# Optimization experiments

Hardware: AMD Instinct MI355X
Metric: run time of the kernel (lower is better)

Reference implementation:

```python
import jax, jax.numpy as jnp
import numpy as np
from jax import lax

# WaveNet constants (canonical values, see shape_source)
AUDIO_C = 256      # AUDIO_CHANNEL_SIZE (mu-law classes)
RES_C   = 64       # ONE_CONV_RESIDUAL_OUT_CHANNELS
FG_C    = 64       # FILTER_GATE_OUT_CHANNELS
SKIP_C  = 256      # ONE_CONV_SKIP_OUT_CHANNELS
K       = 2        # FILTER_GATE_KERNEL_SIZE
BLOCK_N_LAYERS = 10
N_BLOCKS = 2
L = BLOCK_N_LAYERS * N_BLOCKS  # 20 layers
B, T = 4, 16384


def causal_conv(x, w, b, dilation):
    # x: [B,C,T], w: [O,I,K] -> left-padded (causal) dilated conv, output [B,O,T]
    pad = dilation * (K - 1)
    y = lax.conv_general_dilated(x, w, window_strides=(1,), padding=[(pad, 0)],
                                 rhs_dilation=(dilation,),
                                 dimension_numbers=('NCH', 'OIH', 'NCH'))
    return y + b[None, :, None]


def conv1x1(x, w, b):
    # x: [B,C,T], w: [O,C], b: [O]
    return jnp.einsum('oc,bct->bot', w, x) + b[None, :, None]


def setup_inputs() -> dict:
    key = jax.random.key(0)
    ks = jax.random.split(key, 16)
    s = 0.1
    return {
        'x':       jax.random.normal(ks[0], (B, AUDIO_C, T), dtype=jnp.float32),
        'pre_w':   jax.random.normal(ks[1], (RES_C, AUDIO_C), dtype=jnp.float32) * s,
        'pre_b':   jnp.zeros((RES_C,), dtype=jnp.float32),
        'filt_w':  jax.random.normal(ks[2], (L, FG_C, RES_C, K), dtype=jnp.float32) * s,
        'filt_b':  jnp.zeros((L, FG_C), dtype=jnp.float32),
        'gate_w':  jax.random.normal(ks[3], (L, FG_C, RES_C, K), dtype=jnp.float32) * s,
        'gate_b':  jnp.zeros((L, FG_C), dtype=jnp.float32),
        'res_w':   jax.random.normal(ks[4], (L, RES_C, FG_C), dtype=jnp.float32) * s,
        'res_b':   jnp.zeros((L, RES_C), dtype=jnp.float32),
        'skip_w':  jax.random.normal(ks[5], (L, SKIP_C, FG_C), dtype=jnp.float32) * s,
        'skip_b':  jnp.zeros((L, SKIP_C), dtype=jnp.float32),
        'pp1_w':   jax.random.normal(ks[6], (SKIP_C, SKIP_C), dtype=jnp.float32) * s,
        'pp1_b':   jnp.zeros((SKIP_C,), dtype=jnp.float32),
        'pp2_w':   jax.random.normal(ks[7], (AUDIO_C, SKIP_C), dtype=jnp.float32) * s,
        'pp2_b':   jnp.zeros((AUDIO_C,), dtype=jnp.float32),
    }


def reference(x, pre_w, pre_b, filt_w, filt_b, gate_w, gate_b,
              res_w, res_b, skip_w, skip_b, pp1_w, pp1_b, pp2_w, pp2_b):
    h = conv1x1(x, pre_w, pre_b)                       # [B,RES_C,T]
    skip_sum = jnp.zeros((x.shape[0], SKIP_C, x.shape[2]), dtype=x.dtype)
    for i in range(L):                                  # fixed small layer count
        d = 2 ** (i % BLOCK_N_LAYERS)
        wf = causal_conv(h, filt_w[i], filt_b[i], d)
        wg = causal_conv(h, gate_w[i], gate_b[i], d)
        z = jnp.tanh(wf) * jax.nn.sigmoid(wg)           # gated activation unit
        skip_sum = skip_sum + conv1x1(z, skip_w[i], skip_b[i])
        h = h + conv1x1(z, res_w[i], res_b[i])          # residual (dense) stream
    out = conv1x1(jax.nn.relu(skip_sum), pp1_w, pp1_b)  # skip post-processing
    out = conv1x1(jax.nn.relu(out), pp2_w, pp2_b)
    return out                                           # [B,AUDIO_C,T]
```

## Files before the change

kernel.cpp:

```cpp
#include <hip/hip_runtime.h>

#define T_LEN   16384
#define B_SZ    4
#define AUDIO_C 256
#define RES_C   64
#define SKIP_C  256
#define L_LAYERS 20

typedef unsigned short u16;
using bf16x8 = __attribute__((ext_vector_type(8))) __bf16;
using f32x4  = __attribute__((ext_vector_type(4))) float;

__device__ __forceinline__ u16 f2bf(float x){
    union { float f; unsigned u; } v; v.f = x;
    return (u16)((v.u + 0x7FFFu + ((v.u >> 16) & 1u)) >> 16);
}
__device__ __forceinline__ unsigned cvt2(float a, float b){
    union { __bf16 h[2]; unsigned u; } r;
    r.h[0] = (__bf16)a; r.h[1] = (__bf16)b;
    return r.u;
}
__device__ __forceinline__ float bflo(unsigned u){ union{unsigned q; float f;} v; v.q = u << 16; return v.f; }
__device__ __forceinline__ float bfhi(unsigned u){ union{unsigned q; float f;} v; v.q = u & 0xffff0000u; return v.f; }
__device__ __forceinline__ f32x4 mfma16(uint4 a, uint4 b, f32x4 c){
    return __builtin_amdgcn_mfma_f32_16x16x32_bf16(
        __builtin_bit_cast(bf16x8, a), __builtin_bit_cast(bf16x8, b), c, 0, 0, 0);
}
__device__ __forceinline__ int xcd_swz1k(int bid){ return (bid & 7) * 128 + (bid >> 3); }
__device__ __forceinline__ void bar_lgkm(){
    asm volatile("s_waitcnt lgkmcnt(0)" ::: "memory");
    __builtin_amdgcn_s_barrier();
    asm volatile("" ::: "memory");
}

__global__ __launch_bounds__(256) void repack2(
    const float* __restrict__ fw, const float* __restrict__ gw,
    const float* __restrict__ sw, const float* __restrict__ rw,
    const float* __restrict__ p1, const float* __restrict__ p2,
    const float* __restrict__ prw, const float* __restrict__ sb,
    u16* __restrict__ w1p, u16* __restrict__ swp, u16* __restrict__ rwp,
    u16* __restrict__ pp1p, u16* __restrict__ pp2p,
    u16* __restrict__ prep, float* __restrict__ sbsum)
{
    int idx = blockIdx.x * 256 + threadIdx.x;
    if (idx < 327680) {
        int j = idx & 7, l = (idx >> 3) & 63, kk = (idx >> 9) & 3, mt = (idx >> 11) & 7, i = idx >> 14;
        int m = mt * 16 + (l & 15);
        int k = kk * 32 + (l >> 4) * 8 + j;
        const float* srcw = (m < 64) ? fw : gw;
        int mm = m & 63, c = k & 63, tap = k >> 6;
        w1p[idx] = f2bf(srcw[((i * 64 + mm) * 64 + c) * 2 + tap]);
        return;
    }
    idx -= 327680;
    if (idx < 327680) {
        int j = idx & 7, l = (idx >> 3) & 63, kk = (idx >> 9) & 1, mt = (idx >> 10) & 15, i = idx >> 14;
        int p = mt * 16 + (l & 15);
        int c = kk * 32 + (l >> 4) * 8 + j;
        swp[idx] = f2bf(sw[(i * 256 + p) * 64 + c]);
        return;
    }
    idx -= 327680;
    if (idx < 81920) {
        int j = idx & 7, l = (idx >> 3) & 63, kk = (idx >> 9) & 1, mt = (idx >> 10) & 3, i = idx >> 12;
        int o = mt * 16 + (l & 15);
        int c = kk * 32 + (l >> 4) * 8 + j;
        rwp[idx] = f2bf(rw[(i * 64 + o) * 64 + c]);
        return;
    }
    idx -= 81920;
    if (idx < 65536) {
        int j = idx & 7, l = (idx >> 3) & 63, kk = (idx >> 9) & 7, mt = idx >> 12;
        int m = mt * 16 + (l & 15);
        int k = kk * 32 + (l >> 4) * 8 + j;
        pp1p[idx] = f2bf(p1[m * 256 + k]);
        return;
    }
    idx -= 65536;
    if (idx < 65536) {
        int j = idx & 7, l = (idx >> 3) & 63, kk = (idx >> 9) & 7, mt = idx >> 12;
        int m = mt * 16 + (l & 15);
        int k = kk * 32 + (l >> 4) * 8 + j;
        pp2p[idx] = f2bf(p2[m * 256 + k]);
        return;
    }
    idx -= 65536;
    if (idx < 16384) {
        int j = idx & 7, l = (idx >> 3) & 63, kk = (idx >> 9) & 7, mt = idx >> 12;
        int m = mt * 16 + (l & 15);
        int k = kk * 32 + (l >> 4) * 8 + j;
        prep[idx] = f2bf(prw[m * 256 + k]);
        return;
    }
    idx -= 16384;
    if (idx < 256) {
        float s = 0.f;
        for (int i = 0; i < L_LAYERS; ++i) s += sb[i * 256 + idx];
        sbsum[idx] = s;
        return;
    }
}

__global__ __launch_bounds__(256) void pre_mfma(
    const float* __restrict__ x, const u16* __restrict__ prep,
    const float* __restrict__ pre_b, u16* __restrict__ ht)
{
    __shared__ u16 sx[64 * 256];
    unsigned* sx32 = (unsigned*)sx;
    int tid = threadIdx.x;
    int w = tid >> 6, l = tid & 63;
    int lo = l & 15, hi = l >> 4;
    int wg = xcd_swz1k(blockIdx.x);
    int b = wg >> 8, t0 = (wg & 255) * 64;

    const uint4* av = (const uint4*)prep;
    uint4 a[8];
#pragma unroll
    for (int kk = 0; kk < 8; ++kk) a[kk] = av[(w * 8 + kk) * 64 + l];

    {
        int t = l;
        const float* xb = x + (size_t)b * AUDIO_C * T_LEN + t0 + t;
#pragma unroll 8
        for (int c2 = 0; c2 < 64; c2 += 2) {
            int c = w * 64 + c2;
            float v0 = xb[(size_t)c * T_LEN];
            float v1 = xb[(size_t)(c + 1) * T_LEN];
            int ch = c >> 3;
            int a32 = t * 128 + ((ch ^ (t & 7)) << 2) + ((c >> 1) & 3);
            sx32[a32] = cvt2(v0, v1);
        }
    }
    bar_lgkm();

    f32x4 acc[4];
    {
        f32x4 ib;
#pragma unroll
        for (int r = 0; r < 4; ++r) ib[r] = pre_b[w * 16 + hi * 4 + r];
#pragma unroll
        for (int nt = 0; nt < 4; ++nt) acc[nt] = ib;
    }
#pragma unroll
    for (int kk = 0; kk < 8; ++kk) {
#pragma unroll
        for (int nt = 0; nt < 4; ++nt) {
            int t = nt * 16 + lo;
            int ch = kk * 4 + hi;
            uint4 bv = *(const uint4*)&sx32[t * 128 + ((ch ^ (t & 7)) << 2)];
            acc[nt] = mfma16(a[kk], bv, acc[nt]);
        }
    }
#pragma unroll
    for (int nt = 0; nt < 4; ++nt) {
        int t = t0 + nt * 16 + lo;
        uint2 ov;
        ov.x = cvt2(acc[nt][0], acc[nt][1]);
        ov.y = cvt2(acc[nt][2], acc[nt][3]);
        *(uint2*)(ht + ((size_t)b * T_LEN + t) * 64 + w * 16 + hi * 4) = ov;
    }
}

template<int DO_SKIP>
__global__ __launch_bounds__(256) void layer_mfma(
    const u16* __restrict__ htin, u16* __restrict__ htout,
    u16* __restrict__ zTi, float* __restrict__ skipsum,
    const u16* __restrict__ w1p, const u16* __restrict__ swp, const u16* __restrict__ rwp,
    const float* __restrict__ fb, const float* __restrict__ gb,
    const float* __restrict__ sb, const float* __restrict__ rb,
    int d, int first, int last)
{
    __shared__ u16 hl[2 * 64 * 64];
    __shared__ u16 zl[64 * 64];
    int tid = threadIdx.x;
    int w = tid >> 6, l = tid & 63;
    int lo = l & 15, hi = l >> 4;
    int wg = xcd_swz1k(blockIdx.x);
    int b = wg >> 8, t0 = (wg & 255) * 64;
    const u16* hb = htin + (size_t)b * T_LEN * 64;

#pragma unroll
    for (int k = 0; k < 4; ++k) {
        int id = tid + k * 256;
        int region = id >> 9;
        int row = (id >> 3) & 63;
        int g = id & 7;
        int t = region ? (t0 + row) : (t0 - d + row);
        uint4 bv = make_uint4(0u, 0u, 0u, 0u);
        if (t >= 0) bv = *(const uint4*)(hb + (size_t)t * 64 + g * 8);
        *(uint4*)(&hl[(region << 12) + row * 64 + ((g ^ (row & 7)) << 3)]) = bv;
    }

    const uint4* w1v = (const uint4*)w1p;
    uint4 aF[4], aG[4];
#pragma unroll
    for (int kk = 0; kk < 4; ++kk) {
        aF[kk] = w1v[(w * 4 + kk) * 64 + l];
        aG[kk] = w1v[((w + 4) * 4 + kk) * 64 + l];
    }
    uint4 aR[2];
    if (!last) {
        const uint4* rwv = (const uint4*)rwp;
        aR[0] = rwv[(w * 2 + 0) * 64 + l];
        aR[1] = rwv[(w * 2 + 1) * 64 + l];
    }
    f32x4 accF[4], accG[4];
    {
        f32x4 iF, iG;
#pragma unroll
        for (int r = 0; r < 4; ++r) { iF[r] = fb[w * 16 + hi * 4 + r]; iG[r] = gb[w * 16 + hi * 4 + r]; }
#pragma unroll
        for (int nt = 0; nt < 4; ++nt) { accF[nt] = iF; accG[nt] = iG; }
    }
    bar_lgkm();

    __builtin_amdgcn_s_setprio(1);
#pragma unroll
    for (int nt = 0; nt < 4; ++nt) {
        int n = nt * 16 + lo;
#pragma unroll
        for (int kk = 0; kk < 4; ++kk) {
            int gq = (kk & 1) * 4 + hi;
            uint4 bv = *(const uint4*)(&hl[(kk >> 1) * 4096 + n * 64 + ((gq ^ (n & 7)) << 3)]);
            accF[nt] = mfma16(aF[kk], bv, accF[nt]);
            accG[nt] = mfma16(aG[kk], bv, accG[nt]);
        }
    }
    __builtin_amdgcn_s_setprio(0);

#pragma unroll
    for (int nt = 0; nt < 4; ++nt) {
        float zv[4];
#pragma unroll
        for (int r = 0; r < 4; ++r) {
            float f = accF[nt][r], g = accG[nt][r];
            float ef = __expf(2.f * f);
            float th = 1.f - 2.f * __builtin_amdgcn_rcpf(ef + 1.f);
            float sg = __builtin_amdgcn_rcpf(1.f + __expf(-g));
            zv[r] = th * sg;
        }
        int n = nt * 16 + lo;
        int k0 = w * 16 + hi * 4;
        int col = k0 ^ ((n & 7) << 3);
        *(unsigned*)(&zl[n * 64 + col]) = cvt2(zv[0], zv[1]);
        *(unsigned*)(&zl[n * 64 + col + 2]) = cvt2(zv[2], zv[3]);
    }
    bar_lgkm();

    if (!DO_SKIP) {
#pragma unroll
        for (int q = 0; q < 2; ++q) {
            int idx = tid + q * 256;
            int row = idx >> 3, s = idx & 7;
            uint4 v = *(const uint4*)(&zl[row * 64 + ((s ^ (row & 7)) << 3)]);
            *(uint4*)(zTi + ((size_t)b * T_LEN + t0 + row) * 64 + s * 8) = v;
        }
    }

    uint4 aS[4][2];
    f32x4 accS[4][4];
    if (DO_SKIP) {
        const uint4* swv = (const uint4*)swp;
#pragma unroll
        for (int mi = 0; mi < 4; ++mi) {
            aS[mi][0] = swv[((w * 4 + mi) * 2 + 0) * 64 + l];
            aS[mi][1] = swv[((w * 4 + mi) * 2 + 1) * 64 + l];
            f32x4 iS;
#pragma unroll
            for (int r = 0; r < 4; ++r) iS[r] = sb[(w * 4 + mi) * 16 + hi * 4 + r];
#pragma unroll
            for (int nt = 0; nt < 4; ++nt) accS[mi][nt] = iS;
        }
    }
    f32x4 accR[4];
    if (!last) {
        f32x4 iR;
#pragma unroll
        for (int r = 0; r < 4; ++r) iR[r] = rb[w * 16 + hi * 4 + r];
#pragma unroll
        for (int nt = 0; nt < 4; ++nt) accR[nt] = iR;
    }
    __builtin_amdgcn_s_setprio(1);
#pragma unroll
    for (int nt = 0; nt < 4; ++nt) {
        int n = nt * 16 + lo;
#pragma unroll
        for (int kk = 0; kk < 2; ++kk) {
            int kb = kk * 32 + hi * 8;
            uint4 bz = *(const uint4*)(&zl[n * 64 + (kb ^ ((n & 7) << 3))]);
            if (!last) accR[nt] = mfma16(aR[kk], bz, accR[nt]);
            if (DO_SKIP) {
#pragma unroll
                for (int mi = 0; mi < 4; ++mi)
                    accS[mi][nt] = mfma16(aS[mi][kk], bz, accS[mi][nt]);
            }
        }
    }
    __builtin_amdgcn_s_setprio(0);

    if (!last) {
        int ch = w * 2 + (hi >> 1);
        int halfo = (hi & 1) * 4;
#pragma unroll
        for (int nt = 0; nt < 4; ++nt) {
            int n = nt * 16 + lo;
            uint2 hp = *(const uint2*)(&hl[4096 + n * 64 + ((ch ^ (n & 7)) << 3) + halfo]);
            float o0 = bflo(hp.x) + accR[nt][0];
            float o1 = bfhi(hp.x) + accR[nt][1];
            float o2 = bflo(hp.y) + accR[nt][2];
            float o3 = bfhi(hp.y) + accR[nt][3];
            uint2 ov;
            ov.x = cvt2(o0, o1);
            ov.y = cvt2(o2, o3);
            int t = t0 + n;
            *(uint2*)(htout + ((size_t)b * T_LEN + t) * 64 + w * 16 + hi * 4) = ov;
        }
    }
    if (DO_SKIP) {
#pragma unroll
        for (int mi = 0; mi < 4; ++mi) {
#pragma unroll
            for (int nt = 0; nt < 4; ++nt) {
                int t = t0 + nt * 16 + lo;
                int p0 = (w * 4 + mi) * 16 + hi * 4;
#pragma unroll
                for (int r = 0; r < 4; ++r) {
                    float* sp = &skipsum[((size_t)b * 256 + p0 + r) * T_LEN + t];
                    float v = accS[mi][nt][r];
                    if (first) *sp = v; else *sp = *sp + v;
                }
            }
        }
    }
}

#define SP_BODY(L, CUR, OTH, R0, R1)                                            \
    {                                                                            \
        if ((L) + 1 < L_LAYERS) {                                                \
            u16* zn_ = lds + ((OTH) << 12);                                      \
            *(uint4*)(&zn_[loff0]) = R0;                                         \
            *(uint4*)(&zn_[loff1]) = R1;                                         \
            if ((L) + 3 < L_LAYERS) {                                            \
                const u16* zs_ = zT + ((size_t)(((L) + 3) * 4 + b)) * T_LEN * 64;\
                R0 = *(const uint4*)(zs_ + goff0);                               \
                R1 = *(const uint4*)(zs_ + goff1);                               \
            }                                                                    \
        }                                                                        \
        uint4 a1_[4];                                                            \
        _Pragma("unroll")                                                        \
        for (int mi = 0; mi < 4; ++mi)                                           \
            a1_[mi] = swv[(((L) * 16 + w * 4 + mi) * 2 + 1) * 64 + l];           \
        const u16* zc_ = lds + ((CUR) << 12);                                    \
        __builtin_amdgcn_s_setprio(1);                                           \
        _Pragma("unroll")                                                        \
        for (int nt = 0; nt < 4; ++nt) {                                         \
            int n = nt * 16 + lo;                                                \
            uint4 bz = *(const uint4*)(&zc_[n * 64 + ((hi ^ (n & 7)) << 3)]);    \
            _Pragma("unroll")                                                    \
            for (int mi = 0; mi < 4; ++mi)                                       \
                acc[mi][nt] = mfma16(aP[mi], bz, acc[mi][nt]);                   \
        }                                                                        \
        __builtin_amdgcn_s_setprio(0);                                           \
        if ((L) + 1 < L_LAYERS) {                                                \
            _Pragma("unroll")                                                    \
            for (int mi = 0; mi < 4; ++mi)                                       \
                aP[mi] = swv[((((L) + 1) * 16 + w * 4 + mi) * 2 + 0) * 64 + l];  \
        }                                                                        \
        __builtin_amdgcn_s_setprio(1);                                           \
        _Pragma("unroll")                                                        \
        for (int nt = 0; nt < 4; ++nt) {                                         \
            int n = nt * 16 + lo;                                                \
            uint4 bz = *(const uint4*)(&zc_[n * 64 + (((4 + hi) ^ (n & 7)) << 3)]);\
            _Pragma("unroll")                                                    \
            for (int mi = 0; mi < 4; ++mi)                                       \
                acc[mi][nt] = mfma16(a1_[mi], bz, acc[mi][nt]);                  \
        }                                                                        \
        __builtin_amdgcn_s_setprio(0);                                           \
        bar_lgkm();                                                              \
    }

__global__ __launch_bounds__(256) void skip_post(
    const u16* __restrict__ zT, const u16* __restrict__ swpAll,
    const float* __restrict__ sbsum,
    const u16* __restrict__ pp1p, const float* __restrict__ pp1b,
    const u16* __restrict__ pp2p, const float* __restrict__ pp2b,
    float* __restrict__ out)
{
    __shared__ u16 lds[64 * 256];
    int tid = threadIdx.x;
    int w = tid >> 6, l = tid & 63;
    int lo = l & 15, hi = l >> 4;
    int wg = xcd_swz1k(blockIdx.x);
    int b = wg >> 8, t0 = (wg & 255) * 64;

    int idx0 = w * 128 + l, idx1 = idx0 + 64;
    int row0 = idx0 >> 3, s0 = idx0 & 7;
    int row1 = idx1 >> 3, s1 = idx1 & 7;
    size_t goff0 = ((size_t)t0 + row0) * 64 + s0 * 8;
    size_t goff1 = ((size_t)t0 + row1) * 64 + s1 * 8;
    int loff0 = row0 * 64 + ((s0 ^ (row0 & 7)) << 3);
    int loff1 = row1 * 64 + ((s1 ^ (row1 & 7)) << 3);

    f32x4 acc[4][4];
#pragma unroll
    for (int mi = 0; mi < 4; ++mi) {
        f32x4 iS;
#pragma unroll
        for (int r = 0; r < 4; ++r) iS[r] = sbsum[(w * 4 + mi) * 16 + hi * 4 + r];
#pragma unroll
        for (int nt = 0; nt < 4; ++nt) acc[mi][nt] = iS;
    }

    const uint4* swv = (const uint4*)swpAll;
    {
        const u16* z0 = zT + (size_t)b * T_LEN * 64;
        uint4 p0 = *(const uint4*)(z0 + goff0);
        uint4 p1_ = *(const uint4*)(z0 + goff1);
        *(uint4*)(&lds[loff0]) = p0;
        *(uint4*)(&lds[loff1]) = p1_;
    }
    const u16* z1 = zT + ((size_t)4 + b) * T_LEN * 64;
    uint4 rA0 = *(const uint4*)(z1 + goff0);
    uint4 rA1 = *(const uint4*)(z1 + goff1);
    const u16* z2p = zT + ((size_t)(2 * 4 + b)) * T_LEN * 64;
    uint4 rB0 = *(const uint4*)(z2p + goff0);
    uint4 rB1 = *(const uint4*)(z2p + goff1);
    uint4 aP[4];
#pragma unroll
    for (int mi = 0; mi < 4; ++mi)
        aP[mi] = swv[((w * 4 + mi) * 2 + 0) * 64 + l];
    bar_lgkm();

    for (int i = 0; i < L_LAYERS; i += 2) {
        SP_BODY(i,     0, 1, rA0, rA1);
        SP_BODY(i + 1, 1, 0, rB0, rB1);
    }

#pragma unroll
    for (int mi = 0; mi < 4; ++mi) {
#pragma unroll
        for (int nt = 0; nt < 4; ++nt) {
            int n = nt * 16 + lo;
            int k0 = (w * 4 + mi) * 16 + hi * 4;
            int col = k0 ^ ((n & 15) << 3);
            float v0 = acc[mi][nt][0], v1 = acc[mi][nt][1], v2 = acc[mi][nt][2], v3 = acc[mi][nt][3];
            v0 = v0 > 0.f ? v0 : 0.f; v1 = v1 > 0.f ? v1 : 0.f;
            v2 = v2 > 0.f ? v2 : 0.f; v3 = v3 > 0.f ? v3 : 0.f;
            *(unsigned*)(&lds[n * 256 + col]) = cvt2(v0, v1);
            *(unsigned*)(&lds[n * 256 + col + 2]) = cvt2(v2, v3);
        }
    }
    __syncthreads();

    f32x4 u[4][4];
#pragma unroll
    for (int mi = 0; mi < 4; ++mi) {
        f32x4 iU;
#pragma unroll
        for (int r = 0; r < 4; ++r) iU[r] = pp1b[(w * 4 + mi) * 16 + hi * 4 + r];
#pragma unroll
        for (int nt = 0; nt < 4; ++nt) u[mi][nt] = iU;
    }
    {
        const uint4* p1v = (const uint4*)pp1p;
#pragma unroll
        for (int kk = 0; kk < 8; ++kk) {
            uint4 a[4];
#pragma unroll
            for (int mi = 0; mi < 4; ++mi)
                a[mi] = p1v[((w * 4 + mi) * 8 + kk) * 64 + l];
#pragma unroll
            for (int nt = 0; nt < 4; ++nt) {
                int n = nt * 16 + lo;
                int kb = kk * 32 + hi * 8;
                uint4 bz = *(const uint4*)(&lds[n * 256 + (kb ^ ((n & 15) << 3))]);
#pragma unroll
                for (int mi = 0; mi < 4; ++mi)
                    u[mi][nt] = mfma16(a[mi], bz, u[mi][nt]);
            }
        }
    }
    __syncthreads();
#pragma unroll
    for (int mi = 0; mi < 4; ++mi) {
#pragma unroll
        for (int nt = 0; nt < 4; ++nt) {
            int n = nt * 16 + lo;
            int k0 = (w * 4 + mi) * 16 + hi * 4;
            int col = k0 ^ ((n & 15) << 3);
            float v0 = u[mi][nt][0], v1 = u[mi][nt][1], v2 = u[mi][nt][2], v3 = u[mi][nt][3];
            v0 = v0 > 0.f ? v0 : 0.f; v1 = v1 > 0.f ? v1 : 0.f;
            v2 = v2 > 0.f ? v2 : 0.f; v3 = v3 > 0.f ? v3 : 0.f;
            *(unsigned*)(&lds[n * 256 + col]) = cvt2(v0, v1);
            *(unsigned*)(&lds[n * 256 + col + 2]) = cvt2(v2, v3);
        }
    }
    __syncthreads();

    f32x4 vv[4][4];
#pragma unroll
    for (int mi = 0; mi < 4; ++mi) {
        f32x4 iV;
#pragma unroll
        for (int r = 0; r < 4; ++r) iV[r] = pp2b[(w * 4 + mi) * 16 + hi * 4 + r];
#pragma unroll
        for (int nt = 0; nt < 4; ++nt) vv[mi][nt] = iV;
    }
    {
        const uint4* p2v = (const uint4*)pp2p;
#pragma unroll
        for (int kk = 0; kk < 8; ++kk) {
            uint4 a[4];
#pragma unroll
            for (int mi = 0; mi < 4; ++mi)
                a[mi] = p2v[((w * 4 + mi) * 8 + kk) * 64 + l];
#pragma unroll
            for (int nt = 0; nt < 4; ++nt) {
                int n = nt * 16 + lo;
                int kb = kk * 32 + hi * 8;
                uint4 bz = *(const uint4*)(&lds[n * 256 + (kb ^ ((n & 15) << 3))]);
#pragma unroll
                for (int mi = 0; mi < 4; ++mi)
                    vv[mi][nt] = mfma16(a[mi], bz, vv[mi][nt]);
            }
        }
    }
#pragma unroll
    for (int mi = 0; mi < 4; ++mi) {
#pragma unroll
        for (int nt = 0; nt < 4; ++nt) {
            int t = t0 + nt * 16 + lo;
            int p0 = (w * 4 + mi) * 16 + hi * 4;
#pragma unroll
            for (int r = 0; r < 4; ++r)
                out[((size_t)b * 256 + p0 + r) * T_LEN + t] = vv[mi][nt][r];
        }
    }
}

__global__ __launch_bounds__(256) void post_mfma(
    const float* __restrict__ skipsum,
    const u16* __restrict__ pp1p, const float* __restrict__ pp1b,
    const u16* __restrict__ pp2p, const float* __restrict__ pp2b,
    float* __restrict__ out)
{
    __shared__ u16 sl[64 * 256];
    int tid = threadIdx.x;
    int w = tid >> 6, l = tid & 63;
    int lo = l & 15, hi = l >> 4;
    int nblk = T_LEN / 64;
    int b = blockIdx.x / nblk, t0 = (blockIdx.x % nblk) * 64;

#pragma unroll
    for (int mi = 0; mi < 4; ++mi) {
#pragma unroll
        for (int nt = 0; nt < 4; ++nt) {
            int n = nt * 16 + lo;
            int t = t0 + n;
            int p0 = (w * 4 + mi) * 16 + hi * 4;
            float v[4];
#pragma unroll
            for (int r = 0; r < 4; ++r) {
                float s = skipsum[((size_t)b * 256 + p0 + r) * T_LEN + t];
                v[r] = s > 0.f ? s : 0.f;
            }
            int col = p0 ^ ((n & 15) << 3);
            *(unsigned*)(&sl[n * 256 + col]) = cvt2(v[0], v[1]);
            *(unsigned*)(&sl[n * 256 + col + 2]) = cvt2(v[2], v[3]);
        }
    }
    __syncthreads();

    f32x4 u[4][4];
#pragma unroll
    for (int mi = 0; mi < 4; ++mi) {
        f32x4 iU;
#pragma unroll
        for (int r = 0; r < 4; ++r) iU[r] = pp1b[(w * 4 + mi) * 16 + hi * 4 + r];
#pragma unroll
        for (int nt = 0; nt < 4; ++nt) u[mi][nt] = iU;
    }
    {
        const uint4* p1v = (const uint4*)pp1p;
#pragma unroll
        for (int kk = 0; kk < 8; ++kk) {
            uint4 a[4];
#pragma unroll
            for (int mi = 0; mi < 4; ++mi)
                a[mi] = p1v[((w * 4 + mi) * 8 + kk) * 64 + l];
#pragma unroll
            for (int nt = 0; nt < 4; ++nt) {
                int n = nt * 16 + lo;
                int kb = kk * 32 + hi * 8;
                uint4 bz = *(const uint4*)(&sl[n * 256 + (kb ^ ((n & 15) << 3))]);
#pragma unroll
                for (int mi = 0; mi < 4; ++mi)
                    u[mi][nt] = mfma16(a[mi], bz, u[mi][nt]);
            }
        }
    }
    __syncthreads();
#pragma unroll
    for (int mi = 0; mi < 4; ++mi) {
#pragma unroll
        for (int nt = 0; nt < 4; ++nt) {
            int n = nt * 16 + lo;
            int k0 = (w * 4 + mi) * 16 + hi * 4;
            int col = k0 ^ ((n & 15) << 3);
            float v0 = u[mi][nt][0], v1 = u[mi][nt][1], v2 = u[mi][nt][2], v3 = u[mi][nt][3];
            v0 = v0 > 0.f ? v0 : 0.f; v1 = v1 > 0.f ? v1 : 0.f;
            v2 = v2 > 0.f ? v2 : 0.f; v3 = v3 > 0.f ? v3 : 0.f;
            *(unsigned*)(&sl[n * 256 + col]) = cvt2(v0, v1);
            *(unsigned*)(&sl[n * 256 + col + 2]) = cvt2(v2, v3);
        }
    }
    __syncthreads();

    f32x4 vv[4][4];
#pragma unroll
    for (int mi = 0; mi < 4; ++mi) {
        f32x4 iV;
#pragma unroll
        for (int r = 0; r < 4; ++r) iV[r] = pp2b[(w * 4 + mi) * 16 + hi * 4 + r];
#pragma unroll
        for (int nt = 0; nt < 4; ++nt) vv[mi][nt] = iV;
    }
    {
        const uint4* p2v = (const uint4*)pp2p;
#pragma unroll
        for (int kk = 0; kk < 8; ++kk) {
            uint4 a[4];
#pragma unroll
            for (int mi = 0; mi < 4; ++mi)
                a[mi] = p2v[((w * 4 + mi) * 8 + kk) * 64 + l];
#pragma unroll
            for (int nt = 0; nt < 4; ++nt) {
                int n = nt * 16 + lo;
                int kb = kk * 32 + hi * 8;
                uint4 bz = *(const uint4*)(&sl[n * 256 + (kb ^ ((n & 15) << 3))]);
#pragma unroll
                for (int mi = 0; mi < 4; ++mi)
                    vv[mi][nt] = mfma16(a[mi], bz, vv[mi][nt]);
            }
        }
    }
#pragma unroll
    for (int mi = 0; mi < 4; ++mi) {
#pragma unroll
        for (int nt = 0; nt < 4; ++nt) {
            int t = t0 + nt * 16 + lo;
            int p0 = (w * 4 + mi) * 16 + hi * 4;
#pragma unroll
            for (int r = 0; r < 4; ++r)
                out[((size_t)b * 256 + p0 + r) * T_LEN + t] = vv[mi][nt][r];
        }
    }
}

extern "C" void kernel_launch(void* const* d_in, const int* in_sizes, int n_in,
                              void* d_out, int out_size, void* d_ws, size_t ws_size,
                              hipStream_t stream)
{
    const float* x      = (const float*)d_in[0];
    const float* pre_w  = (const float*)d_in[1];
    const float* pre_b  = (const float*)d_in[2];
    const float* filt_w = (const float*)d_in[3];
    const float* filt_b = (const float*)d_in[4];
    const float* gate_w = (const float*)d_in[5];
    const float* gate_b = (const float*)d_in[6];
    const float* res_w  = (const float*)d_in[7];
    const float* res_b  = (const float*)d_in[8];
    const float* skip_w = (const float*)d_in[9];
    const float* skip_b = (const float*)d_in[10];
    const float* pp1_w  = (const float*)d_in[11];
    const float* pp1_b  = (const float*)d_in[12];
    const float* pp2_w  = (const float*)d_in[13];
    const float* pp2_b  = (const float*)d_in[14];
    float* outp = (float*)d_out;

    u16* ht0 = (u16*)outp;
    u16* ht1 = ht0 + (size_t)B_SZ * T_LEN * 64;

    const size_t ZT_BYTES   = (size_t)L_LAYERS * B_SZ * T_LEN * 64 * 2;
    const size_t SKIP_BYTES = (size_t)B_SZ * SKIP_C * T_LEN * 4;

    const bool useZ = ws_size >= ZT_BYTES + (size_t)2 * 1024 * 1024;

    char* ws = (char*)d_ws;
    u16*   zT      = (u16*)ws;
    float* skipsum = (float*)ws;
    size_t packoff = useZ ? ZT_BYTES : SKIP_BYTES;
    u16* w1p  = (u16*)(ws + packoff);
    u16* swp  = w1p + 327680;
    u16* rwp  = swp + 327680;
    u16* pp1p = rwp + 81920;
    u16* pp2p = pp1p + 65536;
    u16* prep = pp2p + 65536;
    float* sbsum = (float*)(prep + 16384);

    repack2<<<3457, 256, 0, stream>>>(filt_w, gate_w, skip_w, res_w, pp1_w, pp2_w, pre_w, skip_b,
                                      w1p, swp, rwp, pp1p, pp2p, prep, sbsum);

    pre_mfma<<<1024, 256, 0, stream>>>(x, prep, pre_b, ht0);

    const u16* hi_ = ht0; u16* ho_ = ht1;
    for (int i = 0; i < L_LAYERS; ++i) {
        int d = 1 << (i % 10);
        int first = (i == 0) ? 1 : 0;
        int last  = (i == L_LAYERS - 1) ? 1 : 0;
        if (useZ)
            layer_mfma<0><<<1024, 256, 0, stream>>>(
                hi_, ho_,
                zT + (size_t)i * 4194304, skipsum,
                w1p + (size_t)i * 16384, swp + (size_t)i * 16384, rwp + (size_t)i * 4096,
                filt_b + i * 64, gate_b + i * 64, skip_b + i * 256, res_b + i * 64,
                d, first, last);
        else
            layer_mfma<1><<<1024, 256, 0, stream>>>(
                hi_, ho_,
                zT, skipsum,
                w1p + (size_t)i * 16384, swp + (size_t)i * 16384, rwp + (size_t)i * 4096,
                filt_b + i * 64, gate_b + i * 64, skip_b + i * 256, res_b + i * 64,
                d, first, last);
        { const u16* tf = hi_; hi_ = ho_; ho_ = (u16*)tf; }
    }

    if (useZ)
        skip_post<<<1024, 256, 0, stream>>>(zT, swp, sbsum, pp1p, pp1_b, pp2p, pp2_b, outp);
    else
        post_mfma<<<1024, 256, 0, stream>>>(skipsum, pp1p, pp1_b, pp2p, pp2_b, outp);
}
```

Baseline: 283.1 us.

## Stage skip_post weights and z through async global-to-LDS multi-buffered pipeline

skip_post now copies each layer's skip weights and z tiles straight into LDS with global_load_lds. It uses a double buffer for weights and a four-deep ring for z, and gates each step with explicit vmcnt waits and a barrier. This replaces register-staged prefetch and per-wave global weight loads. To make the direct copy possible, layer_mfma now writes z to global memory in the already-swizzled LDS layout. The kernel now needs 96KB of dynamic LDS, which lowers occupancy per CU and may require a launch attribute on some runtimes.

```diff
diff --git a/kernel.cpp b/kernel.cpp
--- a/kernel.cpp
+++ b/kernel.cpp
@@ -31,6 +31,11 @@
     asm volatile("s_waitcnt lgkmcnt(0)" ::: "memory");
     __builtin_amdgcn_s_barrier();
     asm volatile("" ::: "memory");
+}
+__device__ __forceinline__ void gload16(const void* g, void* l){
+    __builtin_amdgcn_global_load_lds(
+        (const __attribute__((address_space(1))) void*)g,
+        (__attribute__((address_space(3))) void*)l, 16, 0, 0);
 }
 
 __global__ __launch_bounds__(256) void repack2(
@@ -248,12 +253,11 @@
     bar_lgkm();
 
     if (!DO_SKIP) {
+        u16* zt = zTi + ((size_t)b * T_LEN + t0) * 64;
 #pragma unroll
         for (int q = 0; q < 2; ++q) {
             int idx = tid + q * 256;
-            int row = idx >> 3, s = idx & 7;
-            uint4 v = *(const uint4*)(&zl[row * 64 + ((s ^ (row & 7)) << 3)]);
-            *(uint4*)(zTi + ((size_t)b * T_LEN + t0 + row) * 64 + s * 8) = v;
+            *(uint4*)(zt + idx * 8) = *(const uint4*)(&zl[idx * 8]);
         }
     }
 
@@ -334,49 +338,49 @@
     }
 }
 
-#define SP_BODY(L, CUR, OTH, R0, R1)                                            \
+#define WSTAGE(L)                                                                \
+    if ((L) < L_LAYERS) {                                                        \
+        const u16* gw_ = swpAll + (size_t)(L) * 16384 + w * 4096 + l * 8;        \
+        u16* lw_ = lds + (((L) & 1) * 16384) + w * 4096;                         \
+        _Pragma("unroll")                                                        \
+        for (int j_ = 0; j_ < 8; ++j_)                                           \
+            gload16(gw_ + j_ * 512, lw_ + j_ * 512);                             \
+    }
+#define ZSTAGE(L)                                                                \
+    if ((L) < L_LAYERS) {                                                        \
+        const u16* gz_ = zT + (size_t)(L) * 4194304 + zgbase + w * 1024 + l * 8; \
+        u16* lz_ = lds + 32768 + (((L) & 3) * 4096) + w * 1024;                  \
+        gload16(gz_, lz_);                                                       \
+        gload16(gz_ + 512, lz_ + 512);                                           \
+    }
+#define SPB(L, VCSTR)                                                            \
     {                                                                            \
-        if ((L) + 1 < L_LAYERS) {                                                \
-            u16* zn_ = lds + ((OTH) << 12);                                      \
-            *(uint4*)(&zn_[loff0]) = R0;                                         \
-            *(uint4*)(&zn_[loff1]) = R1;                                         \
-            if ((L) + 3 < L_LAYERS) {                                            \
-                const u16* zs_ = zT + ((size_t)(((L) + 3) * 4 + b)) * T_LEN * 64;\
-                R0 = *(const uint4*)(zs_ + goff0);                               \
-                R1 = *(const uint4*)(zs_ + goff1);                               \
-            }                                                                    \
-        }                                                                        \
-        uint4 a1_[4];                                                            \
+        WSTAGE((L) + 1)                                                          \
+        ZSTAGE((L) + 2)                                                          \
+        asm volatile("s_waitcnt vmcnt(" VCSTR ")" ::: "memory");                 \
+        __builtin_amdgcn_s_barrier();                                            \
+        asm volatile("" ::: "memory");                                           \
+        const u16* zb_ = lds + 32768 + (((L) & 3) * 4096);                       \
+        const u16* wb_ = lds + (((L) & 1) * 16384) + w * 4096;                   \
+        uint4 wf_[4][2];                                                         \
         _Pragma("unroll")                                                        \
-        for (int mi = 0; mi < 4; ++mi)                                           \
-            a1_[mi] = swv[(((L) * 16 + w * 4 + mi) * 2 + 1) * 64 + l];           \
-        const u16* zc_ = lds + ((CUR) << 12);                                    \
-        __builtin_amdgcn_s_setprio(1);                                           \
-        _Pragma("unroll")                                                        \
-        for (int nt = 0; nt < 4; ++nt) {                                         \
-            int n = nt * 16 + lo;                                                \
-            uint4 bz = *(const uint4*)(&zc_[n * 64 + ((hi ^ (n & 7)) << 3)]);    \
-            _Pragma("unroll")                                                    \
-            for (int mi = 0; mi < 4; ++mi)                                       \
-                acc[mi][nt] = mfma16(aP[mi], bz, acc[mi][nt]);                   \
-        }                                                                        \
-        __builtin_amdgcn_s_setprio(0);                                           \
-        if ((L) + 1 < L_LAYERS) {                                                \
-            _Pragma("unroll")                                                    \
-            for (int mi = 0; mi < 4; ++mi)                                       \
-                aP[mi] = swv[((((L) + 1) * 16 + w * 4 + mi) * 2 + 0) * 64 + l];  \
+        for (int mi = 0; mi < 4; ++mi) {                                         \
+            wf_[mi][0] = *(const uint4*)(wb_ + ((mi * 2 + 0) * 64 + l) * 8);     \
+            wf_[mi][1] = *(const uint4*)(wb_ + ((mi * 2 + 1) * 64 + l) * 8);     \
         }                                                                        \
         __builtin_amdgcn_s_setprio(1);                                           \
         _Pragma("unroll")                                                        \
         for (int nt = 0; nt < 4; ++nt) {                                         \
             int n = nt * 16 + lo;                                                \
-            uint4 bz = *(const uint4*)(&zc_[n * 64 + (((4 + hi) ^ (n & 7)) << 3)]);\
+            uint4 bz0 = *(const uint4*)(zb_ + n * 64 + ((hi ^ (n & 7)) << 3));   \
+            uint4 bz1 = *(const uint4*)(zb_ + n * 64 + (((4 + hi) ^ (n & 7)) << 3)); \
             _Pragma("unroll")                                                    \
-            for (int mi = 0; mi < 4; ++mi)                                       \
-                acc[mi][nt] = mfma16(a1_[mi], bz, acc[mi][nt]);                  \
+            for (int mi = 0; mi < 4; ++mi) {                                     \
+                acc[mi][nt] = mfma16(wf_[mi][0], bz0, acc[mi][nt]);              \
+                acc[mi][nt] = mfma16(wf_[mi][1], bz1, acc[mi][nt]);              \
+            }                                                                    \
         }                                                                        \
         __builtin_amdgcn_s_setprio(0);                                           \
-        bar_lgkm();                                                              \
     }
 
 __global__ __launch_bounds__(256) void skip_post(
@@ -386,20 +390,13 @@
     const u16* __restrict__ pp2p, const float* __restrict__ pp2b,
     float* __restrict__ out)
 {
-    __shared__ u16 lds[64 * 256];
+    extern __shared__ u16 lds[];
     int tid = threadIdx.x;
     int w = tid >> 6, l = tid & 63;
     int lo = l & 15, hi = l >> 4;
     int wg = xcd_swz1k(blockIdx.x);
     int b = wg >> 8, t0 = (wg & 255) * 64;
-
-    int idx0 = w * 128 + l, idx1 = idx0 + 64;
-    int row0 = idx0 >> 3, s0 = idx0 & 7;
-    int row1 = idx1 >> 3, s1 = idx1 & 7;
-    size_t goff0 = ((size_t)t0 + row0) * 64 + s0 * 8;
-    size_t goff1 = ((size_t)t0 + row1) * 64 + s1 * 8;
-    int loff0 = row0 * 64 + ((s0 ^ (row0 & 7)) << 3);
-    int loff1 = row1 * 64 + ((s1 ^ (row1 & 7)) << 3);
+    size_t zgbase = ((size_t)b * T_LEN + t0) * 64;
 
     f32x4 acc[4][4];
 #pragma unroll
@@ -411,30 +408,16 @@
         for (int nt = 0; nt < 4; ++nt) acc[mi][nt] = iS;
     }
 
-    const uint4* swv = (const uint4*)swpAll;
-    {
-        const u16* z0 = zT + (size_t)b * T_LEN * 64;
-        uint4 p0 = *(const uint4*)(z0 + goff0);
-        uint4 p1_ = *(const uint4*)(z0 + goff1);
-        *(uint4*)(&lds[loff0]) = p0;
-        *(uint4*)(&lds[loff1]) = p1_;
-    }
-    const u16* z1 = zT + ((size_t)4 + b) * T_LEN * 64;
-    uint4 rA0 = *(const uint4*)(z1 + goff0);
-    uint4 rA1 = *(const uint4*)(z1 + goff1);
-    const u16* z2p = zT + ((size_t)(2 * 4 + b)) * T_LEN * 64;
-    uint4 rB0 = *(const uint4*)(z2p + goff0);
-    uint4 rB1 = *(const uint4*)(z2p + goff1);
-    uint4 aP[4];
-#pragma unroll
-    for (int mi = 0; mi < 4; ++mi)
-        aP[mi] = swv[((w * 4 + mi) * 2 + 0) * 64 + l];
-    bar_lgkm();
-
-    for (int i = 0; i < L_LAYERS; i += 2) {
-        SP_BODY(i,     0, 1, rA0, rA1);
-        SP_BODY(i + 1, 1, 0, rB0, rB1);
-    }
+    WSTAGE(0)
+    ZSTAGE(0)
+    ZSTAGE(1)
+
+    SPB(0,  "12") SPB(1,  "12") SPB(2,  "12") SPB(3,  "12") SPB(4,  "12")
+    SPB(5,  "12") SPB(6,  "12") SPB(7,  "12") SPB(8,  "12") SPB(9,  "12")
+    SPB(10, "12") SPB(11, "12") SPB(12, "12") SPB(13, "12") SPB(14, "12")
+    SPB(15, "12") SPB(16, "12") SPB(17, "12") SPB(18, "10") SPB(19, "0")
+
+    __syncthreads();
 
 #pragma unroll
     for (int mi = 0; mi < 4; ++mi) {
@@ -726,7 +709,7 @@
     }
 
     if (useZ)
-        skip_post<<<1024, 256, 0, stream>>>(zT, swp, sbsum, pp1p, pp1_b, pp2p, pp2_b, outp);
+        skip_post<<<1024, 256, 98304, stream>>>(zT, swp, sbsum, pp1p, pp1_b, pp2p, pp2_b, outp);
     else
         post_mfma<<<1024, 256, 0, stream>>>(skipsum, pp1p, pp1_b, pp2p, pp2_b, outp);
 }
```

Measured after the change: 322.4 us (median of 2 runs). +13.9%, slower.
